# Performance work log

Hardware: AMD Instinct MI355X
Metric: run time of the kernel (lower is better)

Reference implementation:

```python
import jax, jax.numpy as jnp
import numpy as np

C_M, C_Z, C, N_HEAD = 256, 128, 32, 8
N_SEQ, N_RES = 256, 256
LN_EPS = 1e-5


def _layer_norm(x, w, b):
    mu = jnp.mean(x, axis=-1, keepdims=True)
    var = jnp.var(x, axis=-1, keepdims=True)
    return (x - mu) * jax.lax.rsqrt(var + LN_EPS) * w + b


def setup_inputs() -> dict:
    key = jax.random.key(0)
    ks = jax.random.split(key, 12)
    s = 0.02
    return {
        "m": jax.random.normal(ks[0], (N_SEQ, N_RES, C_M), dtype=jnp.float32),
        "z": jax.random.normal(ks[1], (N_RES, N_RES, C_Z), dtype=jnp.float32),
        "ln_m_w": jnp.ones((C_M,), jnp.float32),
        "ln_m_b": jnp.zeros((C_M,), jnp.float32),
        "ln_z_w": jnp.ones((C_Z,), jnp.float32),
        "ln_z_b": jnp.zeros((C_Z,), jnp.float32),
        "Wz": jax.random.normal(ks[2], (C_Z, N_HEAD), dtype=jnp.float32) * s,
        "Wq": jax.random.normal(ks[3], (C_M, N_HEAD * C), dtype=jnp.float32) * s,
        "Wk": jax.random.normal(ks[4], (C_M, N_HEAD * C), dtype=jnp.float32) * s,
        "Wv": jax.random.normal(ks[5], (C_M, N_HEAD * C), dtype=jnp.float32) * s,
        "Wg": jax.random.normal(ks[6], (C_M, N_HEAD * C), dtype=jnp.float32) * s,
        "bg": jnp.zeros((N_HEAD * C,), jnp.float32),
        "Wo": jax.random.normal(ks[7], (N_HEAD * C, C_M), dtype=jnp.float32) * s,
        "bo": jnp.zeros((C_M,), jnp.float32),
    }


def reference(m, z, ln_m_w, ln_m_b, ln_z_w, ln_z_b, Wz, Wq, Wk, Wv, Wg, bg, Wo, bo):
    S, R, cm = m.shape
    mn = _layer_norm(m, ln_m_w, ln_m_b)            # (S, R, c_m)
    zn = _layer_norm(z, ln_z_w, ln_z_b)            # (R, R, c_z)
    bias = jnp.einsum('qkz,zh->hqk', zn, Wz)       # (H, R, R), pair bias per head

    Wqh = Wq.reshape(cm, N_HEAD, C)
    Wkh = Wk.reshape(cm, N_HEAD, C)
    Wvh = Wv.reshape(cm, N_HEAD, C)
    q = jnp.einsum('srm,mhc->shrc', mn, Wqh)       # (S, H, R, c)
    k = jnp.einsum('srm,mhc->shrc', mn, Wkh)
    v = jnp.einsum('srm,mhc->shrc', mn, Wvh)

    scale = 1.0 / jnp.sqrt(jnp.asarray(C, mn.dtype))
    scores = jnp.einsum('shqc,shkc->shqk', q, k) * scale + bias[None]  # (S, H, R, R)
    attn = jax.nn.softmax(scores, axis=-1)
    o = jnp.einsum('shqk,shkc->shqc', attn, v)     # (S, H, R, c)
    o = o.transpose(0, 2, 1, 3).reshape(S, R, N_HEAD * C)

    g = jax.nn.sigmoid(mn @ Wg + bg)               # gating, (S, R, H*c)
    return (g * o) @ Wo + bo                       # (S, R, c_m)
```

## Files before the change

### kernel.cpp

```cpp
#include <hip/hip_runtime.h>
#include <cmath>

#define NSEQ 256
#define NRES 256
#define CM   256
#define CZ   128
#define NHEAD 8
#define CHD  32
#define NROW 65536

typedef __attribute__((ext_vector_type(8))) short short8;
typedef __attribute__((ext_vector_type(4))) float f32x4;

__device__ __forceinline__ unsigned short f2bf(float x) {
    union { float f; unsigned int u; } v; v.f = x;
    unsigned int u = v.u;
    u += 0x7fffu + ((u >> 16) & 1u);
    return (unsigned short)(u >> 16);
}
__device__ __forceinline__ float bf2f(unsigned short b) {
    union { float f; unsigned int u; } v; v.u = ((unsigned int)b) << 16;
    return v.f;
}

__device__ __forceinline__ void async16(const void* g, void* l) {
    __builtin_amdgcn_global_load_lds(
        (const __attribute__((address_space(1))) unsigned int*)g,
        (__attribute__((address_space(3))) unsigned int*)l, 16, 0, 0);
}

__device__ __forceinline__ void xcd_remap(int& x, int& y) {
    const int nx = gridDim.x, ny = gridDim.y;
    const int b = blockIdx.x + blockIdx.y * nx;
    if ((ny & 7) == 0) {
        const int c = b & 7;
        const int t = b >> 3;
        x = t % nx;
        y = c + 8 * (t / nx);
    } else {
        x = blockIdx.x; y = blockIdx.y;
    }
}

__global__ void __launch_bounds__(64)
ln_m_kernel(const float* __restrict__ m, const float* __restrict__ w,
            const float* __restrict__ b, unsigned short* __restrict__ mbf) {
    const int row = blockIdx.x;
    const int t = threadIdx.x;
    const float* x = m + (size_t)row * CM;
    float4 xv = *(const float4*)(x + t * 4);
    float s  = xv.x + xv.y + xv.z + xv.w;
    float s2 = xv.x * xv.x + xv.y * xv.y + xv.z * xv.z + xv.w * xv.w;
#pragma unroll
    for (int off = 32; off > 0; off >>= 1) {
        s  += __shfl_xor(s, off);
        s2 += __shfl_xor(s2, off);
    }
    const float mu  = s * (1.0f / CM);
    const float var = s2 * (1.0f / CM) - mu * mu;
    const float inv = rsqrtf(var + 1e-5f);
    float4 wv = *(const float4*)(w + t * 4);
    float4 bv = *(const float4*)(b + t * 4);
    ushort4 o4;
    o4.x = f2bf((xv.x - mu) * inv * wv.x + bv.x);
    o4.y = f2bf((xv.y - mu) * inv * wv.y + bv.y);
    o4.z = f2bf((xv.z - mu) * inv * wv.z + bv.z);
    o4.w = f2bf((xv.w - mu) * inv * wv.w + bv.w);
    *(ushort4*)(mbf + (size_t)row * CM + t * 4) = o4;
}

__global__ void __launch_bounds__(64)
ln_z_bias_kernel(const float* __restrict__ z, const float* __restrict__ w,
                 const float* __restrict__ b, const float* __restrict__ Wz,
                 float* __restrict__ bias) {
    const int pair = blockIdx.x;
    const int t = threadIdx.x;
    const float* x = z + (size_t)pair * CZ;
    float2 xv = *(const float2*)(x + t * 2);
    float s  = xv.x + xv.y;
    float s2 = xv.x * xv.x + xv.y * xv.y;
#pragma unroll
    for (int off = 32; off > 0; off >>= 1) {
        s  += __shfl_xor(s, off);
        s2 += __shfl_xor(s2, off);
    }
    const float mu  = s * (1.0f / CZ);
    const float var = s2 * (1.0f / CZ) - mu * mu;
    const float inv = rsqrtf(var + 1e-5f);
    float2 wv = *(const float2*)(w + t * 2);
    float2 bv = *(const float2*)(b + t * 2);
    const float zn0 = (xv.x - mu) * inv * wv.x + bv.x;
    const float zn1 = (xv.y - mu) * inv * wv.y + bv.y;
    float ph[NHEAD];
#pragma unroll
    for (int h = 0; h < NHEAD; h++)
        ph[h] = zn0 * Wz[(2 * t) * NHEAD + h] + zn1 * Wz[(2 * t + 1) * NHEAD + h];
#pragma unroll
    for (int h = 0; h < NHEAD; h++) {
#pragma unroll
        for (int off = 32; off > 0; off >>= 1) ph[h] += __shfl_xor(ph[h], off);
    }
    if (t == 0) {
#pragma unroll
        for (int h = 0; h < NHEAD; h++)
            bias[(size_t)h * NROW + pair] = ph[h];
    }
}

__global__ void __launch_bounds__(256)
wsplit_kernel(const float* __restrict__ Wq, const float* __restrict__ Wk,
              const float* __restrict__ Wv, const float* __restrict__ Wg,
              const float* __restrict__ Wo, unsigned short* __restrict__ wbf) {
    const int n = blockIdx.x;
    const int mat = blockIdx.y;
    const int k = threadIdx.x;
    const float* W = (mat == 0) ? Wq : (mat == 1) ? Wk : (mat == 2) ? Wv
                   : (mat == 3) ? Wg : Wo;
    const float v = W[(size_t)k * 256 + n];
    unsigned short h = f2bf(v);
    unsigned short* hi = wbf + (size_t)mat * 65536;
    hi[(size_t)n * 256 + k] = h;
    if (mat == 4) {
        unsigned short* lo = wbf + (size_t)5 * 65536;
        lo[(size_t)n * 256 + k] = f2bf(v - bf2f(h));
    }
}

__device__ __forceinline__ void gemm128_1p(
    const unsigned short* __restrict__ A_g, const unsigned short* __restrict__ Bt_g,
    int m0, int n0, short* A_s, short* B_s,
    unsigned short* __restrict__ C, const float* __restrict__ bias,
    float alpha, int act) {
    const int tid  = threadIdx.x;
    const int wid  = tid >> 6;
    const int lane = tid & 63;
    const int wm = (wid >> 1) * 64;
    const int wn = (wid & 1) * 64;

    f32x4 acc[4][4];
#pragma unroll
    for (int i = 0; i < 4; i++)
#pragma unroll
        for (int j = 0; j < 4; j++) acc[i][j] = (f32x4){0.f, 0.f, 0.f, 0.f};

    const unsigned short* gmat = (wid < 2) ? A_g : Bt_g;
    short* lmat = (wid < 2) ? A_s : B_s;
    const int brow = (wid < 2) ? m0 : n0;
    const int half = (wid & 1) * 64;
    const int srow = lane >> 2;
    const int skq  = (lane & 3) * 8;

    const int lrow = lane & 15;
    const int lk   = (lane >> 4) * 8;

    for (int k0 = 0; k0 < 256; k0 += 32) {
#pragma unroll
        for (int r = 0; r < 4; r++) {
            const unsigned short* g = gmat + (size_t)(brow + half + r * 16 + srow) * 256 + k0 + skq;
            short* l = lmat + (half + r * 16) * 32;
            async16(g, l);
        }
        __syncthreads();

        short8 ah[4], bh[4];
#pragma unroll
        for (int f = 0; f < 4; f++) {
            ah[f] = *(const short8*)&A_s[(wm + f * 16 + lrow) * 32 + lk];
            bh[f] = *(const short8*)&B_s[(wn + f * 16 + lrow) * 32 + lk];
        }
#pragma unroll
        for (int i = 0; i < 4; i++)
#pragma unroll
            for (int j = 0; j < 4; j++)
                acc[i][j] = __builtin_amdgcn_mfma_f32_16x16x32_bf16(ah[i], bh[j], acc[i][j], 0, 0, 0);
        __syncthreads();
    }

    const int ccol0 = lane & 15;
    const int crow0 = (lane >> 4) * 4;
    float bvv[4];
#pragma unroll
    for (int j = 0; j < 4; j++)
        bvv[j] = bias ? bias[n0 + wn + j * 16 + ccol0] : 0.0f;
#pragma unroll
    for (int i = 0; i < 4; i++) {
#pragma unroll
        for (int r = 0; r < 4; r++) {
            const int row = m0 + wm + i * 16 + crow0 + r;
#pragma unroll
            for (int j = 0; j < 4; j++) {
                const int col = n0 + wn + j * 16 + ccol0;
                float v = acc[i][j][r] * alpha + bvv[j];
                if (act == 1) v = 1.0f / (1.0f + __expf(-v));
                C[(size_t)row * 256 + col] = f2bf(v);
            }
        }
    }
}

__device__ __forceinline__ void gemm128_core(
    const unsigned short* __restrict__ Ahi_g, const unsigned short* __restrict__ Alo_g,
    const unsigned short* __restrict__ Bthi_g, const unsigned short* __restrict__ Btlo_g,
    int m0, int n0,
    short* Ahi_s, short* Alo_s, short* Bhi_s, short* Blo_s,
    float* __restrict__ C, const float* __restrict__ bias,
    float alpha, int act) {
    const int tid  = threadIdx.x;
    const int wid  = tid >> 6;
    const int lane = tid & 63;
    const int wm = (wid >> 1) * 64;
    const int wn = (wid & 1) * 64;

    f32x4 acc[4][4];
#pragma unroll
    for (int i = 0; i < 4; i++)
#pragma unroll
        for (int j = 0; j < 4; j++) acc[i][j] = (f32x4){0.f, 0.f, 0.f, 0.f};

    const unsigned short* gmat = (wid == 0) ? Ahi_g : (wid == 1) ? Alo_g
                                : (wid == 2) ? Bthi_g : Btlo_g;
    short* lmat = (wid == 0) ? Ahi_s : (wid == 1) ? Alo_s
                : (wid == 2) ? Bhi_s : Blo_s;
    const int brow = (wid < 2) ? m0 : n0;
    const int srow = lane >> 2;
    const int skq  = (lane & 3) * 8;

    const int lrow = lane & 15;
    const int lk   = (lane >> 4) * 8;

    for (int k0 = 0; k0 < 256; k0 += 32) {
#pragma unroll
        for (int r = 0; r < 8; r++) {
            const unsigned short* g = gmat + (size_t)(brow + r * 16 + srow) * 256 + k0 + skq;
            short* l = lmat + (r * 16) * 32;
            async16(g, l);
        }
        __syncthreads();

        short8 ah[4], al[4], bh[4], bl[4];
#pragma unroll
        for (int f = 0; f < 4; f++) {
            const int ma = (wm + f * 16 + lrow) * 32 + lk;
            const int na = (wn + f * 16 + lrow) * 32 + lk;
            ah[f] = *(const short8*)&Ahi_s[ma];
            al[f] = *(const short8*)&Alo_s[ma];
            bh[f] = *(const short8*)&Bhi_s[na];
            bl[f] = *(const short8*)&Blo_s[na];
        }
#pragma unroll
        for (int i = 0; i < 4; i++)
#pragma unroll
            for (int j = 0; j < 4; j++) {
                acc[i][j] = __builtin_amdgcn_mfma_f32_16x16x32_bf16(ah[i], bh[j], acc[i][j], 0, 0, 0);
                acc[i][j] = __builtin_amdgcn_mfma_f32_16x16x32_bf16(ah[i], bl[j], acc[i][j], 0, 0, 0);
                acc[i][j] = __builtin_amdgcn_mfma_f32_16x16x32_bf16(al[i], bh[j], acc[i][j], 0, 0, 0);
            }
        __syncthreads();
    }

    const int ccol0 = lane & 15;
    const int crow0 = (lane >> 4) * 4;
    float bvv[4];
#pragma unroll
    for (int j = 0; j < 4; j++)
        bvv[j] = bias ? bias[n0 + wn + j * 16 + ccol0] : 0.0f;
#pragma unroll
    for (int i = 0; i < 4; i++) {
#pragma unroll
        for (int r = 0; r < 4; r++) {
            const int row = m0 + wm + i * 16 + crow0 + r;
#pragma unroll
            for (int j = 0; j < 4; j++) {
                const int col = n0 + wn + j * 16 + ccol0;
                float v = acc[i][j][r] * alpha + bvv[j];
                if (act == 1) v = 1.0f / (1.0f + __expf(-v));
                C[(size_t)row * 256 + col] = v;
            }
        }
    }
}

__global__ void __launch_bounds__(256)
gemm_qkvg_kernel(const unsigned short* __restrict__ A,
                 const unsigned short* __restrict__ wbf,
                 unsigned short* __restrict__ qb, unsigned short* __restrict__ kb,
                 unsigned short* __restrict__ vb, unsigned short* __restrict__ gb,
                 const float* __restrict__ bg, float scale) {
    __shared__ short A_s[128 * 32];
    __shared__ short B_s[128 * 32];
    int bx, by;
    xcd_remap(bx, by);
    const int which = bx >> 1;
    const int n0 = (bx & 1) * 128;
    const int m0 = by * 128;
    const unsigned short* bt = wbf + (size_t)which * 65536;
    unsigned short* C = (which == 0) ? qb : (which == 1) ? kb : (which == 2) ? vb : gb;
    const float alpha = (which == 0) ? scale : 1.0f;
    const float* bias = (which == 3) ? bg : nullptr;
    const int act = (which == 3) ? 1 : 0;
    gemm128_1p(A, bt, m0, n0, A_s, B_s, C, bias, alpha, act);
}

__global__ void __launch_bounds__(256)
gemm_out_kernel(const unsigned short* __restrict__ Ahi, const unsigned short* __restrict__ Alo,
                const unsigned short* __restrict__ wbf, float* __restrict__ C,
                const float* __restrict__ bo) {
    __shared__ short Ahi_s[128 * 32];
    __shared__ short Alo_s[128 * 32];
    __shared__ short Bhi_s[128 * 32];
    __shared__ short Blo_s[128 * 32];
    int bx, by;
    xcd_remap(bx, by);
    const unsigned short* bthi = wbf + (size_t)4 * 65536;
    const unsigned short* btlo = wbf + (size_t)5 * 65536;
    gemm128_core(Ahi, Alo, bthi, btlo, by * 128, bx * 128,
                 Ahi_s, Alo_s, Bhi_s, Blo_s, C, bo, 1.0f, 0);
}

__global__ void __launch_bounds__(256, 2)
attn_mfma_kernel(const unsigned short* __restrict__ q, const unsigned short* __restrict__ k,
                 const unsigned short* __restrict__ v, const float* __restrict__ bias,
                 const unsigned short* __restrict__ g,
                 unsigned short* __restrict__ ohi, unsigned short* __restrict__ olo) {
    const int s = blockIdx.x, h = blockIdx.y;
    __shared__ short Ks[256][40];
    __shared__ short Vs[32][264];
    __shared__ short Ps[4][64][40];
    __shared__ float li_s[4][64];
    const int tid = threadIdx.x;
    const int w = tid >> 6, l = tid & 63;
    const int lg = l >> 4, l15 = l & 15;
    const size_t sbase = (size_t)s * (NRES * CM);

    {
        const int kk0 = tid >> 2;
        const int c8 = (tid & 3) * 8;
#pragma unroll
        for (int r4 = 0; r4 < 4; r4++) {
            const int kk = r4 * 64 + kk0;
            const size_t gi = sbase + (size_t)kk * CM + h * CHD + c8;
            short8 k8 = *(const short8*)(k + gi);
            short8 v8 = *(const short8*)(v + gi);
            *(short8*)&Ks[kk][c8] = k8;
#pragma unroll
            for (int jj = 0; jj < 8; jj++) Vs[c8 + jj][kk] = v8[jj];
        }
    }
    const int wq0 = w * 64;
    short8 qf[4];
#pragma unroll
    for (int mq = 0; mq < 4; mq++)
        qf[mq] = *(const short8*)(q + sbase + (size_t)(wq0 + mq * 16 + l15) * CM + h * CHD + lg * 8);
    __syncthreads();

    f32x4 acco[4][2];
#pragma unroll
    for (int mq = 0; mq < 4; mq++)
#pragma unroll
        for (int nc = 0; nc < 2; nc++) acco[mq][nc] = (f32x4){0.f, 0.f, 0.f, 0.f};
    float lip[4] = {0.f, 0.f, 0.f, 0.f};
    const float* bh = bias + (size_t)h * NROW;

    for (int ch = 0; ch < 8; ch++) {
        const int kb = ch * 32;
        short8 kf[2];
#pragma unroll
        for (int ik = 0; ik < 2; ik++)
            kf[ik] = *(const short8*)&Ks[kb + ik * 16 + l15][lg * 8];
#pragma unroll
        for (int jq = 0; jq < 4; jq++) {
            const int qrow = wq0 + jq * 16 + l15;
#pragma unroll
            for (int ik = 0; ik < 2; ik++) {
                f32x4 sa = (f32x4){0.f, 0.f, 0.f, 0.f};
                sa = __builtin_amdgcn_mfma_f32_16x16x32_bf16(kf[ik], qf[jq], sa, 0, 0, 0);
                const int kkr = ik * 16 + lg * 4;
                float4 bv = *(const float4*)(bh + (size_t)qrow * NRES + kb + kkr);
                float p0 = __expf(sa[0] + bv.x);
                float p1 = __expf(sa[1] + bv.y);
                float p2 = __expf(sa[2] + bv.z);
                float p3 = __expf(sa[3] + bv.w);
                lip[jq] += (p0 + p1) + (p2 + p3);
                ushort4 ps;
                ps.x = f2bf(p0); ps.y = f2bf(p1); ps.z = f2bf(p2); ps.w = f2bf(p3);
                *(ushort4*)&Ps[w][jq * 16 + l15][kkr] = ps;
            }
        }
        short8 pf[4], vf[2];
#pragma unroll
        for (int mq = 0; mq < 4; mq++)
            pf[mq] = *(const short8*)&Ps[w][mq * 16 + l15][lg * 8];
#pragma unroll
        for (int nc = 0; nc < 2; nc++)
            vf[nc] = *(const short8*)&Vs[nc * 16 + l15][kb + lg * 8];
#pragma unroll
        for (int mq = 0; mq < 4; mq++)
#pragma unroll
            for (int nc = 0; nc < 2; nc++)
                acco[mq][nc] = __builtin_amdgcn_mfma_f32_16x16x32_bf16(pf[mq], vf[nc], acco[mq][nc], 0, 0, 0);
    }

#pragma unroll
    for (int jq = 0; jq < 4; jq++) {
        lip[jq] += __shfl_xor(lip[jq], 16);
        lip[jq] += __shfl_xor(lip[jq], 32);
        li_s[w][jq * 16 + l15] = lip[jq];
    }

#pragma unroll
    for (int mq = 0; mq < 4; mq++) {
#pragma unroll
        for (int r = 0; r < 4; r++) {
            const int qrow = wq0 + mq * 16 + lg * 4 + r;
            const float inv = 1.0f / li_s[w][mq * 16 + lg * 4 + r];
            const size_t rb = sbase + (size_t)qrow * CM + h * CHD;
#pragma unroll
            for (int nc = 0; nc < 2; nc++) {
                const int c = nc * 16 + l15;
                const float val = acco[mq][nc][r] * inv * bf2f(g[rb + c]);
                const unsigned short hi = f2bf(val);
                ohi[rb + c] = hi;
                olo[rb + c] = f2bf(val - bf2f(hi));
            }
        }
    }
}

extern "C" void kernel_launch(void* const* d_in, const int* in_sizes, int n_in,
                              void* d_out, int out_size, void* d_ws, size_t ws_size,
                              hipStream_t stream) {
    const float* m    = (const float*)d_in[0];
    const float* z    = (const float*)d_in[1];
    const float* lnmw = (const float*)d_in[2];
    const float* lnmb = (const float*)d_in[3];
    const float* lnzw = (const float*)d_in[4];
    const float* lnzb = (const float*)d_in[5];
    const float* Wz   = (const float*)d_in[6];
    const float* Wq   = (const float*)d_in[7];
    const float* Wk   = (const float*)d_in[8];
    const float* Wv   = (const float*)d_in[9];
    const float* Wg   = (const float*)d_in[10];
    const float* bg   = (const float*)d_in[11];
    const float* Wo   = (const float*)d_in[12];
    const float* bo   = (const float*)d_in[13];
    float* out = (float*)d_out;

    char* wsb = (char*)d_ws;
    const size_t BIASB = (size_t)NHEAD * NROW * 4;
    const size_t WBFB  = (size_t)6 * 65536 * 2;
    float* bias = (float*)wsb;
    unsigned short* wbf = (unsigned short*)(wsb + BIASB);
    char* chunk0 = wsb + BIASB + ((WBFB + 255) & ~(size_t)255);

    const size_t avail = ws_size - (size_t)(chunk0 - wsb);
    int SC = NSEQ;
    while (SC > 1 && (size_t)SC * NRES * CM * 12 > avail) SC >>= 1;
    const size_t CHE = (size_t)SC * NRES * CM;

    unsigned short* qb  = (unsigned short*)chunk0;
    unsigned short* kb  = qb + CHE;
    unsigned short* vb  = kb + CHE;
    unsigned short* gb  = vb + CHE;
    unsigned short* mhi = gb + CHE;
    unsigned short* mlo = mhi + CHE;

    ln_z_bias_kernel<<<NROW, 64, 0, stream>>>(z, lnzw, lnzb, Wz, bias);
    wsplit_kernel<<<dim3(256, 5), 256, 0, stream>>>(Wq, Wk, Wv, Wg, Wo, wbf);

    const int rows = SC * NRES;
    const int mtiles = rows / 128;
    const float scale = 0.17677669529663687f;

    for (int s0 = 0; s0 < NSEQ; s0 += SC) {
        const float* m_c   = m   + (size_t)s0 * NRES * CM;
        float*       out_c = out + (size_t)s0 * NRES * CM;

        ln_m_kernel<<<rows, 64, 0, stream>>>(m_c, lnmw, lnmb, mhi);

        gemm_qkvg_kernel<<<dim3(8, mtiles), 256, 0, stream>>>(
            mhi, wbf, qb, kb, vb, gb, bg, scale);

        attn_mfma_kernel<<<dim3(SC, NHEAD), 256, 0, stream>>>(
            qb, kb, vb, bias, gb, mhi, mlo);

        gemm_out_kernel<<<dim3(2, mtiles), 256, 0, stream>>>(
            mhi, mlo, wbf, out_c, bo);
    }
}
```

Baseline: 375.5 us.

## Keep attention probabilities in registers, pack hi/lo output, transpose pair bias

The attention kernel now feeds exp scores straight from the QK MFMA accumulator layout into a 16x16x16 bf16 MFMA against V. This removes the per-wave LDS staging of P and frees LDS, and occupancy is raised to 4 blocks. The pair bias is pre-transposed by a new kernel so each lane reads bias along its own accumulator layout. The attention output hi/lo bf16 halves are packed into one 32-bit word, and the out-projection GEMM unpacks them with byte perms. The costs are an extra transpose kernel and extra workspace, and the per-lane bias loads are now strided across rows instead of one float4.

```diff
diff --git a/kernel.cpp b/kernel.cpp
--- a/kernel.cpp
+++ b/kernel.cpp
@@ -10,6 +10,7 @@
 #define NROW 65536
 
 typedef __attribute__((ext_vector_type(8))) short short8;
+typedef __attribute__((ext_vector_type(4))) short s16x4;
 typedef __attribute__((ext_vector_type(4))) float f32x4;
 
 __device__ __forceinline__ unsigned short f2bf(float x) {
@@ -105,6 +106,21 @@
         for (int h = 0; h < NHEAD; h++)
             bias[(size_t)h * NROW + pair] = ph[h];
     }
+}
+
+__global__ void __launch_bounds__(256)
+bias_tr_kernel(const float* __restrict__ bq, float* __restrict__ bt) {
+    __shared__ float tile[32][33];
+    const int h = blockIdx.z;
+    const int q0 = blockIdx.y * 32, k0 = blockIdx.x * 32;
+    const int tr = threadIdx.x >> 5, tc = threadIdx.x & 31;
+#pragma unroll
+    for (int i = 0; i < 4; i++)
+        tile[tr + i * 8][tc] = bq[(size_t)h * NROW + (size_t)(q0 + tr + i * 8) * 256 + k0 + tc];
+    __syncthreads();
+#pragma unroll
+    for (int i = 0; i < 4; i++)
+        bt[(size_t)h * NROW + (size_t)(k0 + tr + i * 8) * 256 + q0 + tc] = tile[tc][tr + i * 8];
 }
 
 __global__ void __launch_bounds__(256)
@@ -193,88 +209,6 @@
                 float v = acc[i][j][r] * alpha + bvv[j];
                 if (act == 1) v = 1.0f / (1.0f + __expf(-v));
                 C[(size_t)row * 256 + col] = f2bf(v);
-            }
-        }
-    }
-}
-
-__device__ __forceinline__ void gemm128_core(
-    const unsigned short* __restrict__ Ahi_g, const unsigned short* __restrict__ Alo_g,
-    const unsigned short* __restrict__ Bthi_g, const unsigned short* __restrict__ Btlo_g,
-    int m0, int n0,
-    short* Ahi_s, short* Alo_s, short* Bhi_s, short* Blo_s,
-    float* __restrict__ C, const float* __restrict__ bias,
-    float alpha, int act) {
-    const int tid  = threadIdx.x;
-    const int wid  = tid >> 6;
-    const int lane = tid & 63;
-    const int wm = (wid >> 1) * 64;
-    const int wn = (wid & 1) * 64;
-
-    f32x4 acc[4][4];
-#pragma unroll
-    for (int i = 0; i < 4; i++)
-#pragma unroll
-        for (int j = 0; j < 4; j++) acc[i][j] = (f32x4){0.f, 0.f, 0.f, 0.f};
-
-    const unsigned short* gmat = (wid == 0) ? Ahi_g : (wid == 1) ? Alo_g
-                                : (wid == 2) ? Bthi_g : Btlo_g;
-    short* lmat = (wid == 0) ? Ahi_s : (wid == 1) ? Alo_s
-                : (wid == 2) ? Bhi_s : Blo_s;
-    const int brow = (wid < 2) ? m0 : n0;
-    const int srow = lane >> 2;
-    const int skq  = (lane & 3) * 8;
-
-    const int lrow = lane & 15;
-    const int lk   = (lane >> 4) * 8;
-
-    for (int k0 = 0; k0 < 256; k0 += 32) {
-#pragma unroll
-        for (int r = 0; r < 8; r++) {
-            const unsigned short* g = gmat + (size_t)(brow + r * 16 + srow) * 256 + k0 + skq;
-            short* l = lmat + (r * 16) * 32;
-            async16(g, l);
-        }
-        __syncthreads();
-
-        short8 ah[4], al[4], bh[4], bl[4];
-#pragma unroll
-        for (int f = 0; f < 4; f++) {
-            const int ma = (wm + f * 16 + lrow) * 32 + lk;
-            const int na = (wn + f * 16 + lrow) * 32 + lk;
-            ah[f] = *(const short8*)&Ahi_s[ma];
-            al[f] = *(const short8*)&Alo_s[ma];
-            bh[f] = *(const short8*)&Bhi_s[na];
-            bl[f] = *(const short8*)&Blo_s[na];
-        }
-#pragma unroll
-        for (int i = 0; i < 4; i++)
-#pragma unroll
-            for (int j = 0; j < 4; j++) {
-                acc[i][j] = __builtin_amdgcn_mfma_f32_16x16x32_bf16(ah[i], bh[j], acc[i][j], 0, 0, 0);
-                acc[i][j] = __builtin_amdgcn_mfma_f32_16x16x32_bf16(ah[i], bl[j], acc[i][j], 0, 0, 0);
-                acc[i][j] = __builtin_amdgcn_mfma_f32_16x16x32_bf16(al[i], bh[j], acc[i][j], 0, 0, 0);
-            }
-        __syncthreads();
-    }
-
-    const int ccol0 = lane & 15;
-    const int crow0 = (lane >> 4) * 4;
-    float bvv[4];
-#pragma unroll
-    for (int j = 0; j < 4; j++)
-        bvv[j] = bias ? bias[n0 + wn + j * 16 + ccol0] : 0.0f;
-#pragma unroll
-    for (int i = 0; i < 4; i++) {
-#pragma unroll
-        for (int r = 0; r < 4; r++) {
-            const int row = m0 + wm + i * 16 + crow0 + r;
-#pragma unroll
-            for (int j = 0; j < 4; j++) {
-                const int col = n0 + wn + j * 16 + ccol0;
-                float v = acc[i][j][r] * alpha + bvv[j];
-                if (act == 1) v = 1.0f / (1.0f + __expf(-v));
-                C[(size_t)row * 256 + col] = v;
             }
         }
     }
@@ -302,30 +236,115 @@
 }
 
 __global__ void __launch_bounds__(256)
-gemm_out_kernel(const unsigned short* __restrict__ Ahi, const unsigned short* __restrict__ Alo,
+gemm_out_kernel(const unsigned int* __restrict__ Ap_g,
                 const unsigned short* __restrict__ wbf, float* __restrict__ C,
                 const float* __restrict__ bo) {
-    __shared__ short Ahi_s[128 * 32];
-    __shared__ short Alo_s[128 * 32];
+    __shared__ unsigned int Ap_s[128 * 32];
     __shared__ short Bhi_s[128 * 32];
     __shared__ short Blo_s[128 * 32];
     int bx, by;
     xcd_remap(bx, by);
-    const unsigned short* bthi = wbf + (size_t)4 * 65536;
-    const unsigned short* btlo = wbf + (size_t)5 * 65536;
-    gemm128_core(Ahi, Alo, bthi, btlo, by * 128, bx * 128,
-                 Ahi_s, Alo_s, Bhi_s, Blo_s, C, bo, 1.0f, 0);
-}
-
-__global__ void __launch_bounds__(256, 2)
+    const int m0 = by * 128, n0 = bx * 128;
+    const unsigned short* Bthi_g = wbf + (size_t)4 * 65536;
+    const unsigned short* Btlo_g = wbf + (size_t)5 * 65536;
+
+    const int tid  = threadIdx.x;
+    const int wid  = tid >> 6;
+    const int lane = tid & 63;
+    const int wm = (wid >> 1) * 64;
+    const int wn = (wid & 1) * 64;
+
+    f32x4 acc[4][4];
+#pragma unroll
+    for (int i = 0; i < 4; i++)
+#pragma unroll
+        for (int j = 0; j < 4; j++) acc[i][j] = (f32x4){0.f, 0.f, 0.f, 0.f};
+
+    const int lrow = lane & 15;
+    const int lk   = (lane >> 4) * 8;
+
+    for (int k0 = 0; k0 < 256; k0 += 32) {
+        if (wid < 2) {
+            const int half = wid * 64;
+            const int srow = lane >> 3;
+            const int scol = (lane & 7) * 4;
+#pragma unroll
+            for (int r = 0; r < 8; r++) {
+                const unsigned int* g = Ap_g + (size_t)(m0 + half + r * 8 + srow) * 256 + k0 + scol;
+                unsigned int* l = Ap_s + (half + r * 8) * 32;
+                async16(g, l);
+            }
+        } else {
+            const unsigned short* gmat = (wid == 2) ? Bthi_g : Btlo_g;
+            short* lmat = (wid == 2) ? Bhi_s : Blo_s;
+            const int srow = lane >> 2;
+            const int skq  = (lane & 3) * 8;
+#pragma unroll
+            for (int r = 0; r < 8; r++) {
+                const unsigned short* g = gmat + (size_t)(n0 + r * 16 + srow) * 256 + k0 + skq;
+                short* l = lmat + (r * 16) * 32;
+                async16(g, l);
+            }
+        }
+        __syncthreads();
+
+        short8 ah[4], al[4], bh[4], bl[4];
+#pragma unroll
+        for (int f = 0; f < 4; f++) {
+            const uint4* ap = (const uint4*)&Ap_s[(wm + f * 16 + lrow) * 32 + lk];
+            uint4 a0 = ap[0], a1 = ap[1];
+            union { unsigned int u[4]; short8 s; } uh, ul;
+            uh.u[0] = __builtin_amdgcn_perm(a0.y, a0.x, 0x07060302u);
+            uh.u[1] = __builtin_amdgcn_perm(a0.w, a0.z, 0x07060302u);
+            uh.u[2] = __builtin_amdgcn_perm(a1.y, a1.x, 0x07060302u);
+            uh.u[3] = __builtin_amdgcn_perm(a1.w, a1.z, 0x07060302u);
+            ul.u[0] = __builtin_amdgcn_perm(a0.y, a0.x, 0x05040100u);
+            ul.u[1] = __builtin_amdgcn_perm(a0.w, a0.z, 0x05040100u);
+            ul.u[2] = __builtin_amdgcn_perm(a1.y, a1.x, 0x05040100u);
+            ul.u[3] = __builtin_amdgcn_perm(a1.w, a1.z, 0x05040100u);
+            ah[f] = uh.s; al[f] = ul.s;
+            bh[f] = *(const short8*)&Bhi_s[(wn + f * 16 + lrow) * 32 + lk];
+            bl[f] = *(const short8*)&Blo_s[(wn + f * 16 + lrow) * 32 + lk];
+        }
+#pragma unroll
+        for (int i = 0; i < 4; i++)
+#pragma unroll
+            for (int j = 0; j < 4; j++) {
+                acc[i][j] = __builtin_amdgcn_mfma_f32_16x16x32_bf16(ah[i], bh[j], acc[i][j], 0, 0, 0);
+                acc[i][j] = __builtin_amdgcn_mfma_f32_16x16x32_bf16(ah[i], bl[j], acc[i][j], 0, 0, 0);
+                acc[i][j] = __builtin_amdgcn_mfma_f32_16x16x32_bf16(al[i], bh[j], acc[i][j], 0, 0, 0);
+            }
+        __syncthreads();
+    }
+
+    const int ccol0 = lane & 15;
+    const int crow0 = (lane >> 4) * 4;
+    float bvv[4];
+#pragma unroll
+    for (int j = 0; j < 4; j++)
+        bvv[j] = bo[n0 + wn + j * 16 + ccol0];
+#pragma unroll
+    for (int i = 0; i < 4; i++) {
+#pragma unroll
+        for (int r = 0; r < 4; r++) {
+            const int row = m0 + wm + i * 16 + crow0 + r;
+#pragma unroll
+            for (int j = 0; j < 4; j++) {
+                const int col = n0 + wn + j * 16 + ccol0;
+                C[(size_t)row * 256 + col] = acc[i][j][r] + bvv[j];
+            }
+        }
+    }
+}
+
+__global__ void __launch_bounds__(256, 4)
 attn_mfma_kernel(const unsigned short* __restrict__ q, const unsigned short* __restrict__ k,
-                 const unsigned short* __restrict__ v, const float* __restrict__ bias,
+                 const unsigned short* __restrict__ v, const float* __restrict__ bias_t,
                  const unsigned short* __restrict__ g,
-                 unsigned short* __restrict__ ohi, unsigned short* __restrict__ olo) {
+                 unsigned int* __restrict__ opack) {
     const int s = blockIdx.x, h = blockIdx.y;
     __shared__ short Ks[256][40];
-    __shared__ short Vs[32][264];
-    __shared__ short Ps[4][64][40];
+    __shared__ short Vs[32][268];
     __shared__ float li_s[4][64];
     const int tid = threadIdx.x;
     const int w = tid >> 6, l = tid & 63;
@@ -359,7 +378,7 @@
 #pragma unroll
         for (int nc = 0; nc < 2; nc++) acco[mq][nc] = (f32x4){0.f, 0.f, 0.f, 0.f};
     float lip[4] = {0.f, 0.f, 0.f, 0.f};
-    const float* bh = bias + (size_t)h * NROW;
+    const float* bt = bias_t + (size_t)h * NROW;
 
     for (int ch = 0; ch < 8; ch++) {
         const int kb = ch * 32;
@@ -368,36 +387,35 @@
         for (int ik = 0; ik < 2; ik++)
             kf[ik] = *(const short8*)&Ks[kb + ik * 16 + l15][lg * 8];
 #pragma unroll
-        for (int jq = 0; jq < 4; jq++) {
-            const int qrow = wq0 + jq * 16 + l15;
-#pragma unroll
-            for (int ik = 0; ik < 2; ik++) {
+        for (int ik = 0; ik < 2; ik++) {
+            s16x4 vf[2];
+#pragma unroll
+            for (int nc = 0; nc < 2; nc++)
+                vf[nc] = *(const s16x4*)&Vs[nc * 16 + l15][kb + ik * 16 + lg * 4];
+            const int kk0a = kb + ik * 16 + lg * 4;
+#pragma unroll
+            for (int jq = 0; jq < 4; jq++) {
+                const int qrow = wq0 + jq * 16 + l15;
                 f32x4 sa = (f32x4){0.f, 0.f, 0.f, 0.f};
                 sa = __builtin_amdgcn_mfma_f32_16x16x32_bf16(kf[ik], qf[jq], sa, 0, 0, 0);
-                const int kkr = ik * 16 + lg * 4;
-                float4 bv = *(const float4*)(bh + (size_t)qrow * NRES + kb + kkr);
-                float p0 = __expf(sa[0] + bv.x);
-                float p1 = __expf(sa[1] + bv.y);
-                float p2 = __expf(sa[2] + bv.z);
-                float p3 = __expf(sa[3] + bv.w);
+                const float b0 = bt[(size_t)(kk0a + 0) * 256 + qrow];
+                const float b1 = bt[(size_t)(kk0a + 1) * 256 + qrow];
+                const float b2 = bt[(size_t)(kk0a + 2) * 256 + qrow];
+                const float b3 = bt[(size_t)(kk0a + 3) * 256 + qrow];
+                const float p0 = __expf(sa[0] + b0);
+                const float p1 = __expf(sa[1] + b1);
+                const float p2 = __expf(sa[2] + b2);
+                const float p3 = __expf(sa[3] + b3);
                 lip[jq] += (p0 + p1) + (p2 + p3);
-                ushort4 ps;
-                ps.x = f2bf(p0); ps.y = f2bf(p1); ps.z = f2bf(p2); ps.w = f2bf(p3);
-                *(ushort4*)&Ps[w][jq * 16 + l15][kkr] = ps;
-            }
-        }
-        short8 pf[4], vf[2];
-#pragma unroll
-        for (int mq = 0; mq < 4; mq++)
-            pf[mq] = *(const short8*)&Ps[w][mq * 16 + l15][lg * 8];
-#pragma unroll
-        for (int nc = 0; nc < 2; nc++)
-            vf[nc] = *(const short8*)&Vs[nc * 16 + l15][kb + lg * 8];
-#pragma unroll
-        for (int mq = 0; mq < 4; mq++)
-#pragma unroll
-            for (int nc = 0; nc < 2; nc++)
-                acco[mq][nc] = __builtin_amdgcn_mfma_f32_16x16x32_bf16(pf[mq], vf[nc], acco[mq][nc], 0, 0, 0);
+                s16x4 pa;
+                pa[0] = (short)f2bf(p0); pa[1] = (short)f2bf(p1);
+                pa[2] = (short)f2bf(p2); pa[3] = (short)f2bf(p3);
+#pragma unroll
+                for (int nc = 0; nc < 2; nc++)
+                    acco[jq][nc] = __builtin_amdgcn_mfma_f32_16x16x16bf16_1k(
+                        pa, vf[nc], acco[jq][nc], 0, 0, 0);
+            }
+        }
     }
 
 #pragma unroll
@@ -419,8 +437,8 @@
                 const int c = nc * 16 + l15;
                 const float val = acco[mq][nc][r] * inv * bf2f(g[rb + c]);
                 const unsigned short hi = f2bf(val);
-                ohi[rb + c] = hi;
-                olo[rb + c] = f2bf(val - bf2f(hi));
+                const unsigned short lo = f2bf(val - bf2f(hi));
+                opack[rb + c] = ((unsigned int)hi << 16) | lo;
             }
         }
     }
@@ -448,23 +466,25 @@
     char* wsb = (char*)d_ws;
     const size_t BIASB = (size_t)NHEAD * NROW * 4;
     const size_t WBFB  = (size_t)6 * 65536 * 2;
-    float* bias = (float*)wsb;
-    unsigned short* wbf = (unsigned short*)(wsb + BIASB);
-    char* chunk0 = wsb + BIASB + ((WBFB + 255) & ~(size_t)255);
+    float* bias_qk = (float*)wsb;
+    float* bias_t  = (float*)(wsb + BIASB);
+    unsigned short* wbf = (unsigned short*)(wsb + 2 * BIASB);
+    char* chunk0 = wsb + 2 * BIASB + ((WBFB + 255) & ~(size_t)255);
 
     const size_t avail = ws_size - (size_t)(chunk0 - wsb);
     int SC = NSEQ;
-    while (SC > 1 && (size_t)SC * NRES * CM * 12 > avail) SC >>= 1;
+    while (SC > 1 && (size_t)SC * NRES * CM * 14 > avail) SC >>= 1;
     const size_t CHE = (size_t)SC * NRES * CM;
 
     unsigned short* qb  = (unsigned short*)chunk0;
     unsigned short* kb  = qb + CHE;
     unsigned short* vb  = kb + CHE;
     unsigned short* gb  = vb + CHE;
-    unsigned short* mhi = gb + CHE;
-    unsigned short* mlo = mhi + CHE;
-
-    ln_z_bias_kernel<<<NROW, 64, 0, stream>>>(z, lnzw, lnzb, Wz, bias);
+    unsigned short* mbf = gb + CHE;
+    unsigned int* opk   = (unsigned int*)(mbf + CHE);
+
+    ln_z_bias_kernel<<<NROW, 64, 0, stream>>>(z, lnzw, lnzb, Wz, bias_qk);
+    bias_tr_kernel<<<dim3(8, 8, 8), 256, 0, stream>>>(bias_qk, bias_t);
     wsplit_kernel<<<dim3(256, 5), 256, 0, stream>>>(Wq, Wk, Wv, Wg, Wo, wbf);
 
     const int rows = SC * NRES;
@@ -475,15 +495,15 @@
         const float* m_c   = m   + (size_t)s0 * NRES * CM;
         float*       out_c = out + (size_t)s0 * NRES * CM;
 
-        ln_m_kernel<<<rows, 64, 0, stream>>>(m_c, lnmw, lnmb, mhi);
+        ln_m_kernel<<<rows, 64, 0, stream>>>(m_c, lnmw, lnmb, mbf);
 
         gemm_qkvg_kernel<<<dim3(8, mtiles), 256, 0, stream>>>(
-            mhi, wbf, qb, kb, vb, gb, bg, scale);
+            mbf, wbf, qb, kb, vb, gb, bg, scale);
 
         attn_mfma_kernel<<<dim3(SC, NHEAD), 256, 0, stream>>>(
-            qb, kb, vb, bias, gb, mhi, mlo);
+            qb, kb, vb, bias_t, gb, opk);
 
         gemm_out_kernel<<<dim3(2, mtiles), 256, 0, stream>>>(
-            mhi, mlo, wbf, out_c, bo);
-    }
-}
+            opk, wbf, out_c, bo);
+    }
+}
```

Result: slower. 399.1 us (+6.3%).
